# Kernel tuning notes

Measured on AMD Instinct MI355X. Metric: run time of the kernel, lower is better.

The kernel has to match this reference:

```python
import jax, jax.numpy as jnp
import numpy as np
from jax import lax

C_IN, C_OUT, KH, KW = 8, 8, 3, 3
H, W = 2048, 2048


def setup_inputs() -> dict:
    key = jax.random.key(0)
    k_x, k_w = jax.random.split(key)
    x = jax.random.normal(k_x, (C_IN, H, W), dtype=jnp.float32)
    # kaiming-uniform-ish init, bound = 1/sqrt(fan_in)
    bound = 1.0 / np.sqrt(C_IN * KH * KW)
    weight = jax.random.uniform(k_w, (C_OUT, C_IN, KH, KW), dtype=jnp.float32,
                                minval=-bound, maxval=bound)
    return {"x": x, "weight": weight}


def reference(x, weight):
    # Faithful to Conv2d_mvm_function.forward: valid cross-correlation on a
    # single (C,H,W) image; stride/padding/dilation ignored, bias never added.
    out = lax.conv_general_dilated(
        x[None],                      # (1, C_in, H, W)
        weight,                       # (C_out, C_in, KH, KW)
        window_strides=(1, 1),
        padding="VALID",
        dimension_numbers=("NCHW", "OIHW", "NCHW"),
    )
    return out[0]                     # (C_out, H-KH+1, W-KW+1)
```

## Files before the change

### kernel.cpp

```cpp
#include <hip/hip_runtime.h>


#define H_IN   2048
#define W_IN   2048
#define H_OUT  2046
#define W_OUT  2046
#define CIN    8
#define COUT   8

#define TPR 512

__global__ __launch_bounds__(256)
void conv3x3_kernel(const float* __restrict__ x,
                    const float* __restrict__ w,
                    float* __restrict__ out) {
    const int gtid = blockIdx.x * blockDim.x + threadIdx.x;
    const int oh = gtid / TPR;
    const int tw = gtid - oh * TPR;
    const int ow = tw * 4;
    if (oh >= H_OUT) return;

    const bool full = (ow + 4 <= W_OUT);

    float acc[COUT][4];
    #pragma unroll
    for (int co = 0; co < COUT; ++co)
        #pragma unroll
        for (int p = 0; p < 4; ++p)
            acc[co][p] = 0.0f;

    for (int ci = 0; ci < CIN; ++ci) {
        #pragma unroll
        for (int kh = 0; kh < 3; ++kh) {
            const float* p = x + ((size_t)ci * H_IN + (size_t)(oh + kh)) * W_IN + ow;
            float in[6];
            const float4 v4 = *reinterpret_cast<const float4*>(p);
            in[0] = v4.x; in[1] = v4.y; in[2] = v4.z; in[3] = v4.w;
            if (full) {
                const float2 v2 = *reinterpret_cast<const float2*>(p + 4);
                in[4] = v2.x; in[5] = v2.y;
            } else {
                in[4] = 0.0f; in[5] = 0.0f;
            }
            #pragma unroll
            for (int co = 0; co < COUT; ++co) {
                #pragma unroll
                for (int kw = 0; kw < 3; ++kw) {
                    const float wt = w[((co * CIN + ci) * 3 + kh) * 3 + kw];
                    #pragma unroll
                    for (int px = 0; px < 4; ++px)
                        acc[co][px] = fmaf(wt, in[kw + px], acc[co][px]);
                }
            }
        }
    }

    #pragma unroll
    for (int co = 0; co < COUT; ++co) {
        float* o = out + ((size_t)co * H_OUT + (size_t)oh) * W_OUT + ow;
        *reinterpret_cast<float2*>(o) = make_float2(acc[co][0], acc[co][1]);
        if (full)
            *reinterpret_cast<float2*>(o + 2) = make_float2(acc[co][2], acc[co][3]);
    }
}

extern "C" void kernel_launch(void* const* d_in, const int* in_sizes, int n_in,
                              void* d_out, int out_size, void* d_ws, size_t ws_size,
                              hipStream_t stream) {
    const float* x = (const float*)d_in[0];
    const float* w = (const float*)d_in[1];
    float* out = (float*)d_out;

    const int total_threads = H_OUT * TPR;
    const int block = 256;
    const int grid = (total_threads + block - 1) / block;

    conv3x3_kernel<<<grid, block, 0, stream>>>(x, w, out);
}
```

Baseline: 262.6 us.

## Compute two output rows per thread to reuse input row loads

Each thread now produces two adjacent output rows, loading four input rows per channel instead of three rows per output row. Input reads per output drop from 3 to 2 rows, and each weight load feeds two accumulator sets. The cost is doubled accumulator registers (64 floats), which may lower occupancy, and half as many threads.

```diff
diff --git a/kernel.cpp b/kernel.cpp
--- a/kernel.cpp
+++ b/kernel.cpp
@@ -9,58 +9,76 @@
 #define COUT   8
 
 #define TPR 512
+#define NGROUPS 1023
 
 __global__ __launch_bounds__(256)
-void conv3x3_kernel(const float* __restrict__ x,
-                    const float* __restrict__ w,
-                    float* __restrict__ out) {
-    const int gtid = blockIdx.x * blockDim.x + threadIdx.x;
-    const int oh = gtid / TPR;
-    const int tw = gtid - oh * TPR;
+void conv3x3_v2(const float* __restrict__ x,
+                const float* __restrict__ w,
+                float* __restrict__ out) {
+    const int gtid = blockIdx.x * 256 + threadIdx.x;
+    const int g  = gtid / TPR;
+    const int tw = gtid - g * TPR;
+    const int oh = g * 2;
     const int ow = tw * 4;
-    if (oh >= H_OUT) return;
 
-    const bool full = (ow + 4 <= W_OUT);
+    const bool full = (tw != TPR - 1);
 
-    float acc[COUT][4];
+    float acc[2][COUT][4];
     #pragma unroll
-    for (int co = 0; co < COUT; ++co)
+    for (int r = 0; r < 2; ++r)
         #pragma unroll
-        for (int p = 0; p < 4; ++p)
-            acc[co][p] = 0.0f;
+        for (int co = 0; co < COUT; ++co)
+            #pragma unroll
+            for (int p = 0; p < 4; ++p)
+                acc[r][co][p] = 0.0f;
 
     for (int ci = 0; ci < CIN; ++ci) {
+        float in[4][6];
         #pragma unroll
-        for (int kh = 0; kh < 3; ++kh) {
-            const float* p = x + ((size_t)ci * H_IN + (size_t)(oh + kh)) * W_IN + ow;
-            float in[6];
+        for (int r = 0; r < 4; ++r) {
+            const float* p = x + ((size_t)ci * H_IN + (size_t)(oh + r)) * W_IN + ow;
             const float4 v4 = *reinterpret_cast<const float4*>(p);
-            in[0] = v4.x; in[1] = v4.y; in[2] = v4.z; in[3] = v4.w;
+            in[r][0] = v4.x; in[r][1] = v4.y; in[r][2] = v4.z; in[r][3] = v4.w;
             if (full) {
                 const float2 v2 = *reinterpret_cast<const float2*>(p + 4);
-                in[4] = v2.x; in[5] = v2.y;
+                in[r][4] = v2.x; in[r][5] = v2.y;
             } else {
-                in[4] = 0.0f; in[5] = 0.0f;
+                in[r][4] = 0.0f; in[r][5] = 0.0f;
             }
+        }
+
+        #pragma unroll
+        for (int r = 0; r < 4; ++r) {
             #pragma unroll
             for (int co = 0; co < COUT; ++co) {
                 #pragma unroll
                 for (int kw = 0; kw < 3; ++kw) {
-                    const float wt = w[((co * CIN + ci) * 3 + kh) * 3 + kw];
-                    #pragma unroll
-                    for (int px = 0; px < 4; ++px)
-                        acc[co][px] = fmaf(wt, in[kw + px], acc[co][px]);
+                    if (r < 3) {
+                        const float wt = w[((co * CIN + ci) * 3 + r) * 3 + kw];
+                        #pragma unroll
+                        for (int px = 0; px < 4; ++px)
+                            acc[0][co][px] = fmaf(wt, in[r][kw + px], acc[0][co][px]);
+                    }
+                    if (r >= 1) {
+                        const float wt = w[((co * CIN + ci) * 3 + (r - 1)) * 3 + kw];
+                        #pragma unroll
+                        for (int px = 0; px < 4; ++px)
+                            acc[1][co][px] = fmaf(wt, in[r][kw + px], acc[1][co][px]);
+                    }
                 }
             }
         }
     }
 
     #pragma unroll
-    for (int co = 0; co < COUT; ++co) {
-        float* o = out + ((size_t)co * H_OUT + (size_t)oh) * W_OUT + ow;
-        *reinterpret_cast<float2*>(o) = make_float2(acc[co][0], acc[co][1]);
-        if (full)
-            *reinterpret_cast<float2*>(o + 2) = make_float2(acc[co][2], acc[co][3]);
+    for (int r = 0; r < 2; ++r) {
+        #pragma unroll
+        for (int co = 0; co < COUT; ++co) {
+            float* o = out + ((size_t)co * H_OUT + (size_t)(oh + r)) * W_OUT + ow;
+            *reinterpret_cast<float2*>(o) = make_float2(acc[r][co][0], acc[r][co][1]);
+            if (full)
+                *reinterpret_cast<float2*>(o + 2) = make_float2(acc[r][co][2], acc[r][co][3]);
+        }
     }
 }
 
@@ -71,9 +89,9 @@
     const float* w = (const float*)d_in[1];
     float* out = (float*)d_out;
 
-    const int total_threads = H_OUT * TPR;
+    const int total_threads = NGROUPS * TPR;
     const int block = 256;
-    const int grid = (total_threads + block - 1) / block;
+    const int grid = total_threads / block;
 
-    conv3x3_kernel<<<grid, block, 0, stream>>>(x, w, out);
+    conv3x3_v2<<<grid, block, 0, stream>>>(x, w, out);
 }
```

Measured after the change: 254.3 us. -3.2%, faster.
